# Optimization experiments

Hardware: AMD Instinct MI355X
Metric: run time of the kernel (lower is better)

The kernel has to match this reference:

```python
import jax, jax.numpy as jnp
import numpy as np

GT_POSITIVE_THRESHOLD = 3.0  # pixels, from config['gt_positive_threshold']


def setup_inputs() -> dict:
    key = jax.random.key(0)
    k0, k1, k2 = jax.random.split(key, 3)
    B, N0, N1 = 8, 2048, 2048
    W, H = 640.0, 480.0
    scale = jnp.array([W, H], dtype=jnp.float32)
    kpts0 = jax.random.uniform(k0, (B, N0, 2), dtype=jnp.float32) * scale
    kpts1 = jax.random.uniform(k1, (B, N1, 2), dtype=jnp.float32) * scale
    # near-identity homography per pair (small perturbation keeps points in-frame)
    transformation = (jnp.eye(3, dtype=jnp.float32)[None]
                      + 0.001 * jax.random.normal(k2, (B, 3, 3), dtype=jnp.float32))
    return {"kpts0": kpts0, "kpts1": kpts1, "transformation": transformation}


def _reproject_keypoints(kpts, H):
    # kpts: [B,N,2], H: [B,3,3] homography. Homogeneous projection.
    ones = jnp.ones(kpts.shape[:-1] + (1,), dtype=kpts.dtype)
    pts_h = jnp.concatenate([kpts, ones], axis=-1)           # [B,N,3]
    proj = jnp.einsum('bij,bnj->bni', H, pts_h)              # [B,N,3]
    return proj[..., :2] / (proj[..., 2:3] + 1e-8)


def _cdist(a, b):
    # a: [B,N0,2], b: [B,N1,2] -> [B,N0,N1] Euclidean distances
    a2 = jnp.sum(a * a, axis=-1)                             # [B,N0]
    b2 = jnp.sum(b * b, axis=-1)                             # [B,N1]
    ab = jnp.einsum('bnd,bmd->bnm', a, b)                    # [B,N0,N1]
    d2 = a2[:, :, None] + b2[:, None, :] - 2.0 * ab
    return jnp.sqrt(jnp.maximum(d2, 0.0))


def reference(kpts0, kpts1, transformation):
    B, N0, _ = kpts0.shape
    N1 = kpts1.shape[1]
    kpts0_t = _reproject_keypoints(kpts0, transformation)
    err = _cdist(kpts0_t, kpts1)                             # [B,N0,N1]

    min_dist0 = jnp.min(err, axis=2)                         # [B,N0]
    gt_matches0 = jnp.argmin(err, axis=2).astype(jnp.int32)  # [B,N0]
    gt_matches1 = jnp.argmin(err, axis=1).astype(jnp.int32)  # [B,N1]

    # cross-check: kpts1's best match of kpts0's best match must be the kpt itself
    back = jnp.take_along_axis(gt_matches1, gt_matches0, axis=1)  # [B,N0]
    idx0 = jnp.arange(N0, dtype=jnp.int32)[None, :]
    inconsistent = (back != idx0) | (min_dist0 > GT_POSITIVE_THRESHOLD)
    gt_matches0 = jnp.where(inconsistent, -1, gt_matches0)

    # rebuild inverse map: gt_matches1[b, gt_matches0[b,i]] = i for valid i
    valid = gt_matches0 != -1
    tgt = jnp.where(valid, gt_matches0, N1)                  # N1 is out-of-range -> dropped
    src = jnp.broadcast_to(idx0, (B, N0))
    gt_matches1_out = jnp.full((B, N1), -1, dtype=jnp.int32)
    gt_matches1_out = gt_matches1_out.at[jnp.arange(B)[:, None], tgt].set(src, mode='drop')

    return gt_matches0, gt_matches1_out, min_dist0
```

## Files before the change

kernel.cpp:

```cpp
#include <hip/hip_runtime.h>


#define SPN 2048
#define SPT 16384
#define RPB 16

__device__ __forceinline__ void sp_reproject(const float* __restrict__ T, int b,
                                             float x, float y,
                                             float& X, float& Y, float& S) {
  const float* H = T + b * 9;
  float p0 = __fadd_rn(__fadd_rn(__fmul_rn(H[0], x), __fmul_rn(H[1], y)), H[2]);
  float p1 = __fadd_rn(__fadd_rn(__fmul_rn(H[3], x), __fmul_rn(H[4], y)), H[5]);
  float p2 = __fadd_rn(__fadd_rn(__fmul_rn(H[6], x), __fmul_rn(H[7], y)), H[8]);
  float den = __fadd_rn(p2, 1e-8f);
  X = __fdiv_rn(p0, den);
  Y = __fdiv_rn(p1, den);
  S = __fadd_rn(__fmul_rn(X, X), __fmul_rn(Y, Y));
}

__global__ __launch_bounds__(256) void sp_prep(
    const float2* __restrict__ k0, const float2* __restrict__ k1,
    const float* __restrict__ T, float4* __restrict__ q0, float4* __restrict__ q1) {
  int t = blockIdx.x * 256 + threadIdx.x;
  if (t < SPT) {
    float2 p = k0[t];
    float X, Y, S;
    sp_reproject(T, t >> 11, p.x, p.y, X, Y, S);
    q0[t] = make_float4(X, Y, S, 0.0f);
  } else {
    int u = t - SPT;
    float2 p = k1[u];
    float S = __fadd_rn(__fmul_rn(p.x, p.x), __fmul_rn(p.y, p.y));
    q1[u] = make_float4(p.x, p.y, S, 0.0f);
  }
}

__device__ __forceinline__ void sp_row16(
    const float rx2[RPB], const float ry2[RPB], const float rs[RPB],
    float bv[RPB], int bi[RPB], float4 v, int c) {
#pragma unroll
  for (int r = 0; r < RPB; r++) {
    float ab2 = __fadd_rn(__fmul_rn(rx2[r], v.x), __fmul_rn(ry2[r], v.y));
    float d2 = __fsub_rn(__fadd_rn(rs[r], v.z), ab2);
    float dm = fmaxf(d2, 0.0f);
    if (dm < bv[r]) { bv[r] = dm; bi[r] = c; }
  }
}

__global__ __launch_bounds__(256, 4) void SuperPointMatchesGenerator_56925496541369_kernel(
    const float4* __restrict__ q0, const float4* __restrict__ q1,
    unsigned short* __restrict__ gt0p, unsigned short* __restrict__ gt1,
    float* __restrict__ out_mind) {
  const bool m1 = blockIdx.x >= (SPT / RPB);
  const int base = (m1 ? blockIdx.x - SPT / RPB : blockIdx.x) * RPB;
  const int b = base >> 11, cb = b << 11;
  const float4* __restrict__ qr = m1 ? q1 : q0;
  const float4* __restrict__ qc = (m1 ? q0 : q1) + cb;

  float rx2[RPB], ry2[RPB], rs[RPB], bv[RPB];
  int bi[RPB];
#pragma unroll
  for (int r = 0; r < RPB; r++) {
    float4 v = qr[base + r];
    rx2[r] = __fadd_rn(v.x, v.x);
    ry2[r] = __fadd_rn(v.y, v.y);
    rs[r] = v.z;
    bv[r] = INFINITY; bi[r] = 0;
  }

#pragma unroll 1
  for (int c = threadIdx.x; c < SPN; c += 512) {
    float4 va = qc[c];
    float4 vb = qc[c + 256];
    sp_row16(rx2, ry2, rs, bv, bi, va, c);
    sp_row16(rx2, ry2, rs, bv, bi, vb, c + 256);
  }

  unsigned long long key[RPB];
#pragma unroll
  for (int r = 0; r < RPB; r++)
    key[r] = ((unsigned long long)__float_as_uint(bv[r]) << 32) | (unsigned)bi[r];
#pragma unroll
  for (int off = 32; off > 0; off >>= 1) {
#pragma unroll
    for (int r = 0; r < RPB; r++) {
      unsigned long long o = __shfl_down(key[r], off);
      if (o < key[r]) key[r] = o;
    }
  }
  __shared__ unsigned long long part[4][RPB];
  if ((threadIdx.x & 63) == 0) {
    int w = threadIdx.x >> 6;
#pragma unroll
    for (int r = 0; r < RPB; r++) part[w][r] = key[r];
  }
  __syncthreads();
  if (threadIdx.x < RPB) {
    int r = threadIdx.x;
    unsigned long long k = part[0][r];
#pragma unroll
    for (int w = 1; w < 4; w++)
      if (part[w][r] < k) k = part[w][r];
    int idx = (int)(k & 0x7ffu);
    if (!m1) {
      float e = __fsqrt_rn(__uint_as_float((unsigned)(k >> 32)));
      unsigned short pk = (unsigned short)idx;
      if (e > 3.0f) pk |= 0x8000u;
      gt0p[base + r] = pk;
      out_mind[base + r] = e;
    } else {
      gt1[base + r] = (unsigned short)idx;
    }
  }
}

__global__ __launch_bounds__(256) void SuperPointMatchesGenerator_56925496541369_final(
    const unsigned short* __restrict__ gt0p, const unsigned short* __restrict__ gt1,
    float* __restrict__ out) {
  int t = blockIdx.x * 256 + threadIdx.x;
  if (t >= SPT) return;
  int b = t >> 11, i = t & 2047, cb = b << 11;

  unsigned short p0 = gt0p[t];
  int m0 = p0 & 0x7ff;
  bool ok0 = ((p0 & 0x8000u) == 0) && ((int)gt1[cb + m0] == i);
  out[t] = ok0 ? (float)m0 : -1.0f;

  int istar = gt1[t];
  unsigned short ps = gt0p[cb + istar];
  bool ok1 = (((int)(ps & 0x7ff)) == i) && ((ps & 0x8000u) == 0);
  out[SPT + t] = ok1 ? (float)istar : -1.0f;
}

__global__ __launch_bounds__(256) void sp_fb_main(
    const float2* __restrict__ k0, const float2* __restrict__ k1,
    const float* __restrict__ T, unsigned short* __restrict__ gt0p,
    unsigned short* __restrict__ gt1, float* __restrict__ out_mind) {
  const bool mode1 = blockIdx.x >= SPN;
  const int base = (mode1 ? blockIdx.x - SPN : blockIdx.x) * 8;
  const int b = base >> 11, cb = b << 11;
  float rx[8], ry[8], rs[8], bv[8];
  int bi[8];
#pragma unroll
  for (int r = 0; r < 8; r++) { bv[r] = INFINITY; bi[r] = 0; }
  if (!mode1) {
#pragma unroll
    for (int r = 0; r < 8; r++) {
      float2 p = k0[base + r];
      sp_reproject(T, b, p.x, p.y, rx[r], ry[r], rs[r]);
    }
    for (int c = threadIdx.x; c < SPN; c += 256) {
      float2 p = k1[cb + c];
      float b2 = __fadd_rn(__fmul_rn(p.x, p.x), __fmul_rn(p.y, p.y));
#pragma unroll
      for (int r = 0; r < 8; r++) {
        float ab = __fadd_rn(__fmul_rn(rx[r], p.x), __fmul_rn(ry[r], p.y));
        float d2 = __fsub_rn(__fadd_rn(rs[r], b2), __fmul_rn(2.0f, ab));
        float dm = fmaxf(d2, 0.0f);
        if (dm < bv[r]) { bv[r] = dm; bi[r] = c; }
      }
    }
  } else {
#pragma unroll
    for (int r = 0; r < 8; r++) {
      float2 p = k1[base + r];
      rx[r] = p.x; ry[r] = p.y;
      rs[r] = __fadd_rn(__fmul_rn(p.x, p.x), __fmul_rn(p.y, p.y));
    }
    for (int c = threadIdx.x; c < SPN; c += 256) {
      float2 p = k0[cb + c];
      float cx, cy, a2;
      sp_reproject(T, b, p.x, p.y, cx, cy, a2);
#pragma unroll
      for (int r = 0; r < 8; r++) {
        float ab = __fadd_rn(__fmul_rn(rx[r], cx), __fmul_rn(ry[r], cy));
        float d2 = __fsub_rn(__fadd_rn(a2, rs[r]), __fmul_rn(2.0f, ab));
        float dm = fmaxf(d2, 0.0f);
        if (dm < bv[r]) { bv[r] = dm; bi[r] = c; }
      }
    }
  }
  unsigned long long key[8];
#pragma unroll
  for (int r = 0; r < 8; r++)
    key[r] = ((unsigned long long)__float_as_uint(bv[r]) << 32) | (unsigned)bi[r];
#pragma unroll
  for (int off = 32; off > 0; off >>= 1) {
#pragma unroll
    for (int r = 0; r < 8; r++) {
      unsigned long long o = __shfl_down(key[r], off);
      if (o < key[r]) key[r] = o;
    }
  }
  __shared__ unsigned long long part[4][8];
  if ((threadIdx.x & 63) == 0) {
    int w = threadIdx.x >> 6;
#pragma unroll
    for (int r = 0; r < 8; r++) part[w][r] = key[r];
  }
  __syncthreads();
  if (threadIdx.x < 8) {
    int r = threadIdx.x;
    unsigned long long k = part[0][r];
#pragma unroll
    for (int w = 1; w < 4; w++)
      if (part[w][r] < k) k = part[w][r];
    int idx = (int)(k & 0x7ffu);
    if (!mode1) {
      float e = __fsqrt_rn(__uint_as_float((unsigned)(k >> 32)));
      unsigned short pk = (unsigned short)idx;
      if (e > 3.0f) pk |= 0x8000u;
      gt0p[base + r] = pk;
      out_mind[base + r] = e;
    } else {
      gt1[base + r] = (unsigned short)idx;
    }
  }
}

extern "C" void kernel_launch(void* const* d_in, const int* in_sizes, int n_in,
                              void* d_out, int out_size, void* d_ws, size_t ws_size,
                              hipStream_t stream) {
  (void)in_sizes; (void)n_in; (void)out_size;
  const float2* k0 = (const float2*)d_in[0];
  const float2* k1 = (const float2*)d_in[1];
  const float* T   = (const float*)d_in[2];
  float* out = (float*)d_out;

  const size_t need = (size_t)2 * SPT * sizeof(float4)
                    + (size_t)2 * SPT * sizeof(unsigned short);
  if (ws_size >= need) {
    float4* q0 = (float4*)d_ws;
    float4* q1 = q0 + SPT;
    unsigned short* gt0p = (unsigned short*)(q1 + SPT);
    unsigned short* gt1  = gt0p + SPT;
    sp_prep<<<2 * SPT / 256, 256, 0, stream>>>(k0, k1, T, q0, q1);
    SuperPointMatchesGenerator_56925496541369_kernel<<<2 * (SPT / RPB), 256, 0, stream>>>(
        q0, q1, gt0p, gt1, out + 2 * SPT);
    SuperPointMatchesGenerator_56925496541369_final<<<SPT / 256, 256, 0, stream>>>(
        gt0p, gt1, out);
  } else {
    unsigned short* gt0p = (unsigned short*)d_ws;
    unsigned short* gt1  = gt0p + SPT;
    sp_fb_main<<<2 * SPN, 256, 0, stream>>>(k0, k1, T, gt0p, gt1, out + 2 * SPT);
    SuperPointMatchesGenerator_56925496541369_final<<<SPT / 256, 256, 0, stream>>>(
        gt0p, gt1, out);
  }
}
```

Measured before the change: 84.90 us.

## Switch keypoint workspace to SoA and use packed float2 math in distance loop

Precomputed keypoint data moves from an AoS float4 layout to separate x, y and squared-norm arrays. The main kernel now reads pairs of columns as 2-wide vectors and does the distance arithmetic on ext_vector float2, which can map to packed FP32 instructions on CDNA. FMA contraction is turned off so results keep the original rounding. The column loop is fully unrolled into four iterations of two columns each, but per-element compare/select still runs scalar.

```diff
diff --git a/kernel.cpp b/kernel.cpp
--- a/kernel.cpp
+++ b/kernel.cpp
@@ -4,6 +4,8 @@
 #define SPN 2048
 #define SPT 16384
 #define RPB 16
+
+typedef float v2f __attribute__((ext_vector_type(2)));
 
 __device__ __forceinline__ void sp_reproject(const float* __restrict__ T, int b,
                                              float x, float y,
@@ -20,60 +22,69 @@
 
 __global__ __launch_bounds__(256) void sp_prep(
     const float2* __restrict__ k0, const float2* __restrict__ k1,
-    const float* __restrict__ T, float4* __restrict__ q0, float4* __restrict__ q1) {
+    const float* __restrict__ T,
+    float* __restrict__ qx0, float* __restrict__ qy0, float* __restrict__ qs0,
+    float* __restrict__ qx1, float* __restrict__ qy1, float* __restrict__ qs1) {
   int t = blockIdx.x * 256 + threadIdx.x;
   if (t < SPT) {
     float2 p = k0[t];
     float X, Y, S;
     sp_reproject(T, t >> 11, p.x, p.y, X, Y, S);
-    q0[t] = make_float4(X, Y, S, 0.0f);
+    qx0[t] = X; qy0[t] = Y; qs0[t] = S;
   } else {
     int u = t - SPT;
     float2 p = k1[u];
-    float S = __fadd_rn(__fmul_rn(p.x, p.x), __fmul_rn(p.y, p.y));
-    q1[u] = make_float4(p.x, p.y, S, 0.0f);
-  }
-}
-
-__device__ __forceinline__ void sp_row16(
-    const float rx2[RPB], const float ry2[RPB], const float rs[RPB],
-    float bv[RPB], int bi[RPB], float4 v, int c) {
-#pragma unroll
-  for (int r = 0; r < RPB; r++) {
-    float ab2 = __fadd_rn(__fmul_rn(rx2[r], v.x), __fmul_rn(ry2[r], v.y));
-    float d2 = __fsub_rn(__fadd_rn(rs[r], v.z), ab2);
-    float dm = fmaxf(d2, 0.0f);
-    if (dm < bv[r]) { bv[r] = dm; bi[r] = c; }
+    qx1[u] = p.x; qy1[u] = p.y;
+    qs1[u] = __fadd_rn(__fmul_rn(p.x, p.x), __fmul_rn(p.y, p.y));
   }
 }
 
 __global__ __launch_bounds__(256, 4) void SuperPointMatchesGenerator_56925496541369_kernel(
-    const float4* __restrict__ q0, const float4* __restrict__ q1,
+    const float* __restrict__ qx0, const float* __restrict__ qy0,
+    const float* __restrict__ qs0, const float* __restrict__ qx1,
+    const float* __restrict__ qy1, const float* __restrict__ qs1,
     unsigned short* __restrict__ gt0p, unsigned short* __restrict__ gt1,
     float* __restrict__ out_mind) {
+#pragma clang fp contract(off)
   const bool m1 = blockIdx.x >= (SPT / RPB);
   const int base = (m1 ? blockIdx.x - SPT / RPB : blockIdx.x) * RPB;
   const int b = base >> 11, cb = b << 11;
-  const float4* __restrict__ qr = m1 ? q1 : q0;
-  const float4* __restrict__ qc = (m1 ? q0 : q1) + cb;
+  const float* __restrict__ rxa = m1 ? qx1 : qx0;
+  const float* __restrict__ rya = m1 ? qy1 : qy0;
+  const float* __restrict__ rsa = m1 ? qs1 : qs0;
+  const float* __restrict__ cxa = (m1 ? qx0 : qx1) + cb;
+  const float* __restrict__ cya = (m1 ? qy0 : qy1) + cb;
+  const float* __restrict__ csa = (m1 ? qs0 : qs1) + cb;
 
   float rx2[RPB], ry2[RPB], rs[RPB], bv[RPB];
   int bi[RPB];
 #pragma unroll
   for (int r = 0; r < RPB; r++) {
-    float4 v = qr[base + r];
-    rx2[r] = __fadd_rn(v.x, v.x);
-    ry2[r] = __fadd_rn(v.y, v.y);
-    rs[r] = v.z;
+    float x = rxa[base + r], y = rya[base + r];
+    rx2[r] = __fadd_rn(x, x);
+    ry2[r] = __fadd_rn(y, y);
+    rs[r] = rsa[base + r];
     bv[r] = INFINITY; bi[r] = 0;
   }
 
-#pragma unroll 1
-  for (int c = threadIdx.x; c < SPN; c += 512) {
-    float4 va = qc[c];
-    float4 vb = qc[c + 256];
-    sp_row16(rx2, ry2, rs, bv, bi, va, c);
-    sp_row16(rx2, ry2, rs, bv, bi, vb, c + 256);
+  const v2f vzero = {0.0f, 0.0f};
+#pragma unroll
+  for (int k = 0; k < 4; k++) {
+    const int c = 2 * (int)threadIdx.x + 512 * k;
+    v2f cx = *(const v2f*)(cxa + c);
+    v2f cy = *(const v2f*)(cya + c);
+    v2f cs = *(const v2f*)(csa + c);
+#pragma unroll
+    for (int r = 0; r < RPB; r++) {
+      v2f t1 = rx2[r] * cx;
+      v2f t2 = ry2[r] * cy;
+      v2f ab2 = t1 + t2;
+      v2f ss = rs[r] + cs;
+      v2f d2 = ss - ab2;
+      v2f dm = __builtin_elementwise_max(d2, vzero);
+      if (dm.x < bv[r]) { bv[r] = dm.x; bi[r] = c; }
+      if (dm.y < bv[r]) { bv[r] = dm.y; bi[r] = c + 1; }
+    }
   }
 
   unsigned long long key[RPB];
@@ -227,16 +238,20 @@
   const float* T   = (const float*)d_in[2];
   float* out = (float*)d_out;
 
-  const size_t need = (size_t)2 * SPT * sizeof(float4)
+  const size_t need = (size_t)6 * SPT * sizeof(float)
                     + (size_t)2 * SPT * sizeof(unsigned short);
   if (ws_size >= need) {
-    float4* q0 = (float4*)d_ws;
-    float4* q1 = q0 + SPT;
-    unsigned short* gt0p = (unsigned short*)(q1 + SPT);
+    float* qx0 = (float*)d_ws;
+    float* qy0 = qx0 + SPT;
+    float* qs0 = qy0 + SPT;
+    float* qx1 = qs0 + SPT;
+    float* qy1 = qx1 + SPT;
+    float* qs1 = qy1 + SPT;
+    unsigned short* gt0p = (unsigned short*)(qs1 + SPT);
     unsigned short* gt1  = gt0p + SPT;
-    sp_prep<<<2 * SPT / 256, 256, 0, stream>>>(k0, k1, T, q0, q1);
+    sp_prep<<<2 * SPT / 256, 256, 0, stream>>>(k0, k1, T, qx0, qy0, qs0, qx1, qy1, qs1);
     SuperPointMatchesGenerator_56925496541369_kernel<<<2 * (SPT / RPB), 256, 0, stream>>>(
-        q0, q1, gt0p, gt1, out + 2 * SPT);
+        qx0, qy0, qs0, qx1, qy1, qs1, gt0p, gt1, out + 2 * SPT);
     SuperPointMatchesGenerator_56925496541369_final<<<SPT / 256, 256, 0, stream>>>(
         gt0p, gt1, out);
   } else {
```

Result: no change. 86.49 us (+1.9%).
